# Performance work log

Hardware: AMD Instinct MI355X
Metric: run time of the kernel (lower is better)

The kernel has to match this reference:

```python
import jax, jax.numpy as jnp
import numpy as np

CAUSAL = True

def setup_inputs() -> dict:
    key = jax.random.key(0)
    kq, kk, kv = jax.random.split(key, 3)
    B, S, H, D = 2, 2048, 16, 64
    q = jax.random.normal(kq, (B, S, H, D), dtype=jnp.float32)
    k = jax.random.normal(kk, (B, S, H, D), dtype=jnp.float32)
    v = jax.random.normal(kv, (B, S, H, D), dtype=jnp.float32)
    return {"q": q, "k": k, "v": v}

def reference(q, k, v):
    # q,k,v: [B, S, H, D]
    B, Sq, H, D = q.shape
    Sk = k.shape[1]
    scale = 1.0 / jnp.sqrt(jnp.asarray(D, dtype=q.dtype))
    # scores: [B, H, Sq, Sk]
    scores = jnp.einsum('bqhd,bkhd->bhqk', q * scale, k)
    if CAUSAL:
        causal_mask = jnp.triu(jnp.ones((Sq, Sk), dtype=bool), k=1)
        scores = jnp.where(causal_mask, -jnp.inf, scores)
    attn = jax.nn.softmax(scores, axis=-1)
    # output: [B, Sq, H, D]
    out = jnp.einsum('bhqk,bkhd->bqhd', attn, v)
    return out
```

## Files before the change

### kernel.cpp

```cpp
#include <hip/hip_runtime.h>


typedef __bf16  bf16x8_t  __attribute__((ext_vector_type(8)));
typedef short   short8_t  __attribute__((ext_vector_type(8)));
typedef float   f32x4     __attribute__((ext_vector_type(4)));

#define MFMA_K32(a, b, c) __builtin_amdgcn_mfma_f32_16x16x32_bf16((a), (b), (c), 0, 0, 0)
#define BC8(x) __builtin_bit_cast(bf16x8_t, (x))

constexpr int   SEQ = 2048, NH = 16;
constexpr int   SROW = NH * 64;
constexpr float QS   = 0.125f * 1.44269504088896f;

__device__ __forceinline__ unsigned f2bfu(float f) {
    unsigned u = __builtin_bit_cast(unsigned, f);
    return (u + 0x7fffu + ((u >> 16) & 1u)) >> 16;
}
__device__ __forceinline__ unsigned pk2(float x, float y) {
#if defined(__HIP_DEVICE_COMPILE__) && __has_builtin(__builtin_amdgcn_cvt_pk_bf16_f32)
    typedef __bf16 bfv2 __attribute__((ext_vector_type(2)));
    bfv2 v = __builtin_amdgcn_cvt_pk_bf16_f32(x, y);
    return __builtin_bit_cast(unsigned, v);
#else
    return (f2bfu(x) & 0xffffu) | (f2bfu(y) << 16);
#endif
}

__global__ __launch_bounds__(256) void prepack(const float* __restrict__ K,
                                               const float* __restrict__ V,
                                               unsigned short* __restrict__ Kp,
                                               unsigned short* __restrict__ Vp) {
    const int blk = blockIdx.x;
    const int tid = threadIdx.x;
    const int bh = blk >> 5, c = blk & 31;
    const int b  = bh >> 4,  h = bh & 15;

    __shared__ float LK[64][68];
    __shared__ float LV[64][68];

    const float* Ksrc = K + (size_t)(b * SEQ + c * 64) * SROW + h * 64;
    const float* Vsrc = V + (size_t)(b * SEQ + c * 64) * SROW + h * 64;

#pragma unroll
    for (int p = 0; p < 4; ++p) {
        const int f   = p * 256 + tid;
        const int row = f >> 4;
        const int c4  = (f & 15) * 4;
        float4 kk = *(const float4*)(Ksrc + (size_t)row * SROW + c4);
        float4 vv = *(const float4*)(Vsrc + (size_t)row * SROW + c4);
        *(float4*)&LK[row][c4] = kk;
        *(float4*)&LV[row][c4] = vv;
    }
    __syncthreads();

#pragma unroll
    for (int u = tid; u < 512; u += 256) {
        const int q_l = u >> 7, ks = (u >> 6) & 1, lane = u & 63;
        const int lhi = lane >> 4, llo = lane & 15;
        const float* r = &LK[q_l * 16 + llo][ks * 32 + lhi * 8];
        uint4 o;
        o.x = pk2(r[0], r[1]); o.y = pk2(r[2], r[3]);
        o.z = pk2(r[4], r[5]); o.w = pk2(r[6], r[7]);
        *(uint4*)(Kp + (size_t)(bh * 128 + c * 4) * 1024 + u * 8) = o;
    }

#pragma unroll
    for (int u = tid; u < 512; u += 256) {
        const int g_l = u >> 8, dt = (u >> 6) & 3, lane = u & 63;
        const int lhi = lane >> 4, llo = lane & 15;
        const int d   = dt * 16 + llo;
        const int kvb = g_l * 32 + lhi * 4;
        uint4 o;
        o.x = pk2(LV[kvb + 0][d],  LV[kvb + 1][d]);
        o.y = pk2(LV[kvb + 2][d],  LV[kvb + 3][d]);
        o.z = pk2(LV[kvb + 16][d], LV[kvb + 17][d]);
        o.w = pk2(LV[kvb + 18][d], LV[kvb + 19][d]);
        *(uint4*)(Vp + (size_t)(bh * 64 + c * 2) * 2048 + u * 8) = o;
    }
}

__global__ __launch_bounds__(256, 4) void fa_fwd(const float* __restrict__ Q,
                                                 const unsigned short* __restrict__ Kp,
                                                 const unsigned short* __restrict__ Vp,
                                                 float* __restrict__ O) {
    const int id = blockIdx.x;
    const int bh = id & 31;
    const int T  = 63 - (id >> 5);
    const int b  = bh >> 4, h = bh & 15;
    const int NSC = (T + 4) >> 2;
    const int q0  = T * 32;

    const int tid  = threadIdx.x;
    const int w    = tid >> 6;
    const int lane = tid & 63;
    const int lhi  = lane >> 4;
    const int llo  = lane & 15;

    __shared__ __align__(16) float Red[4][5][64][4];

    const char* Ku = (const char*)Kp + ((size_t)bh << 18);
    const char* Vu = (const char*)Vp + ((size_t)bh << 18);
    int kov = (w << 12) + lane * 16;
    int vov = (w << 12) + lane * 16;

    bf16x8_t qf[2][2];
#pragma unroll
    for (int mt = 0; mt < 2; ++mt)
#pragma unroll
        for (int ks = 0; ks < 2; ++ks) {
            const float* qp = Q + (size_t)(b * SEQ + q0 + mt * 16 + llo) * SROW + h * 64 + ks * 32 + lhi * 8;
            float4 a = ((const float4*)qp)[0], c4 = ((const float4*)qp)[1];
            uint4 u;
            u.x = pk2(a.x * QS, a.y * QS); u.y = pk2(a.z * QS, a.w * QS);
            u.z = pk2(c4.x * QS, c4.y * QS); u.w = pk2(c4.z * QS, c4.w * QS);
            qf[mt][ks] = __builtin_bit_cast(bf16x8_t, u);
        }

    f32x4 acc[2][4], accL[2];
#pragma unroll
    for (int mt = 0; mt < 2; ++mt) {
        accL[mt] = (f32x4){0.f, 0.f, 0.f, 0.f};
#pragma unroll
        for (int dt = 0; dt < 4; ++dt) acc[mt][dt] = (f32x4){0.f, 0.f, 0.f, 0.f};
    }

    short8_t o8;
#pragma unroll
    for (int j = 0; j < 8; ++j) o8[j] = (short)0x3F80;
    const bf16x8_t ones8 = __builtin_bit_cast(bf16x8_t, o8);

    uint4 kc[4];
#pragma unroll
    for (int i = 0; i < 4; ++i) kc[i] = *(const uint4*)(Ku + kov + i * 1024);

    for (int sc = 0; sc < NSC; ++sc) {
        uint4 vc[4];
#pragma unroll
        for (int dt = 0; dt < 4; ++dt) vc[dt] = *(const uint4*)(Vu + vov + dt * 1024);

        const int kb = (sc << 7) + (w << 5);

        __builtin_amdgcn_s_setprio(1);
        f32x4 s00 = (f32x4){0.f, 0.f, 0.f, 0.f};
        f32x4 s01 = (f32x4){0.f, 0.f, 0.f, 0.f};
        f32x4 s10 = (f32x4){0.f, 0.f, 0.f, 0.f};
        f32x4 s11 = (f32x4){0.f, 0.f, 0.f, 0.f};
        s00 = MFMA_K32(BC8(kc[0]), qf[0][0], s00);
        s10 = MFMA_K32(BC8(kc[0]), qf[1][0], s10);
        s01 = MFMA_K32(BC8(kc[2]), qf[0][0], s01);
        s11 = MFMA_K32(BC8(kc[2]), qf[1][0], s11);
        s00 = MFMA_K32(BC8(kc[1]), qf[0][1], s00);
        s10 = MFMA_K32(BC8(kc[1]), qf[1][1], s10);
        s01 = MFMA_K32(BC8(kc[3]), qf[0][1], s01);
        s11 = MFMA_K32(BC8(kc[3]), qf[1][1], s11);
        __builtin_amdgcn_s_setprio(0);

        kov += 16384;
#pragma unroll
        for (int i = 0; i < 4; ++i) kc[i] = *(const uint4*)(Ku + kov + i * 1024);

        {
            const int m_g0 = q0 + llo;
            if (kb + 15 > q0) {
#pragma unroll
                for (int r = 0; r < 4; ++r)
                    if (kb + lhi * 4 + r > m_g0) s00[r] = -INFINITY;
            }
            if (kb + 31 > q0) {
#pragma unroll
                for (int r = 0; r < 4; ++r)
                    if (kb + 16 + lhi * 4 + r > m_g0) s01[r] = -INFINITY;
            }
            const int m1  = q0 + 16;
            const int m_g1 = m1 + llo;
            if (kb + 15 > m1) {
#pragma unroll
                for (int r = 0; r < 4; ++r)
                    if (kb + lhi * 4 + r > m_g1) s10[r] = -INFINITY;
            }
            if (kb + 31 > m1) {
#pragma unroll
                for (int r = 0; r < 4; ++r)
                    if (kb + 16 + lhi * 4 + r > m_g1) s11[r] = -INFINITY;
            }
        }

        uint4 up0, up1;
        up0.x = pk2(__builtin_amdgcn_exp2f(s00[0]), __builtin_amdgcn_exp2f(s00[1]));
        up0.y = pk2(__builtin_amdgcn_exp2f(s00[2]), __builtin_amdgcn_exp2f(s00[3]));
        up0.z = pk2(__builtin_amdgcn_exp2f(s01[0]), __builtin_amdgcn_exp2f(s01[1]));
        up0.w = pk2(__builtin_amdgcn_exp2f(s01[2]), __builtin_amdgcn_exp2f(s01[3]));
        up1.x = pk2(__builtin_amdgcn_exp2f(s10[0]), __builtin_amdgcn_exp2f(s10[1]));
        up1.y = pk2(__builtin_amdgcn_exp2f(s10[2]), __builtin_amdgcn_exp2f(s10[3]));
        up1.z = pk2(__builtin_amdgcn_exp2f(s11[0]), __builtin_amdgcn_exp2f(s11[1]));
        up1.w = pk2(__builtin_amdgcn_exp2f(s11[2]), __builtin_amdgcn_exp2f(s11[3]));
        const bf16x8_t pf0 = BC8(up0);
        const bf16x8_t pf1 = BC8(up1);

        __builtin_amdgcn_s_setprio(1);
#pragma unroll
        for (int dt = 0; dt < 4; ++dt) {
            acc[0][dt] = MFMA_K32(pf0, BC8(vc[dt]), acc[0][dt]);
            acc[1][dt] = MFMA_K32(pf1, BC8(vc[dt]), acc[1][dt]);
        }
        accL[0] = MFMA_K32(pf0, ones8, accL[0]);
        accL[1] = MFMA_K32(pf1, ones8, accL[1]);
        __builtin_amdgcn_s_setprio(0);

        vov += 16384;
    }

#pragma unroll
    for (int mt = 0; mt < 2; ++mt) {
#pragma unroll
        for (int dt = 0; dt < 4; ++dt) *(f32x4*)&Red[w][dt][lane][0] = acc[mt][dt];
        *(f32x4*)&Red[w][4][lane][0] = accL[mt];
        __syncthreads();
        f32x4 oc = (f32x4){0.f, 0.f, 0.f, 0.f};
        f32x4 ls = (f32x4){0.f, 0.f, 0.f, 0.f};
#pragma unroll
        for (int u = 0; u < 4; ++u) {
            oc += *(const f32x4*)&Red[u][w][lane][0];
            ls += *(const f32x4*)&Red[u][4][lane][0];
        }
#pragma unroll
        for (int r = 0; r < 4; ++r)
            O[(size_t)(b * SEQ + q0 + mt * 16 + lhi * 4 + r) * SROW + h * 64 + w * 16 + llo] = oc[r] / ls[r];
        __syncthreads();
    }
}

extern "C" void kernel_launch(void* const* d_in, const int* in_sizes, int n_in,
                              void* d_out, int out_size, void* d_ws, size_t ws_size,
                              hipStream_t stream) {
    const float* q = (const float*)d_in[0];
    const float* k = (const float*)d_in[1];
    const float* v = (const float*)d_in[2];
    float* o = (float*)d_out;
    unsigned short* Kp = (unsigned short*)d_ws;
    unsigned short* Vp = Kp + (size_t)32 * 32 * 4096;
    prepack<<<dim3(1024), dim3(256), 0, stream>>>(k, v, Kp, Vp);
    fa_fwd<<<dim3(2048), dim3(256), 0, stream>>>(q, Kp, Vp, o);
}
```

Before: 123.6 us.

## Stage K/V tiles in LDS via async global_load_lds double buffering with warp-split work

Replaces per-wave direct register loads of K/V with block-wide async global-to-LDS loads into a double-buffered shared tile, so each 64-key chunk is fetched once per block and shared by all four waves. Waves are re-split as two query m-tiles times two key halves, which halves per-wave register state, so the occupancy hint is raised from 4 to 5. Waves whose rows are fully masked skip the work, and the final reduction reuses the LDS buffer and multiplies by a reciprocal. It adds a __syncthreads per iteration and smaller per-iteration work, which risks sync overhead, and the prefetch on the last iteration reads one chunk past the end.

```diff
diff --git a/kernel.cpp b/kernel.cpp
--- a/kernel.cpp
+++ b/kernel.cpp
@@ -23,6 +23,14 @@
     return __builtin_bit_cast(unsigned, v);
 #else
     return (f2bfu(x) & 0xffffu) | (f2bfu(y) << 16);
+#endif
+}
+
+__device__ __forceinline__ void gload_lds16(const void* g, void* l) {
+#if defined(__HIP_DEVICE_COMPILE__)
+    __builtin_amdgcn_global_load_lds(
+        (const __attribute__((address_space(1))) unsigned*)g,
+        (__attribute__((address_space(3))) unsigned*)l, 16, 0, 0);
 #endif
 }
 
@@ -79,7 +87,7 @@
     }
 }
 
-__global__ __launch_bounds__(256, 4) void fa_fwd(const float* __restrict__ Q,
+__global__ __launch_bounds__(256, 5) void fa_fwd(const float* __restrict__ Q,
                                                  const unsigned short* __restrict__ Kp,
                                                  const unsigned short* __restrict__ Vp,
                                                  float* __restrict__ O) {
@@ -87,146 +95,141 @@
     const int bh = id & 31;
     const int T  = 63 - (id >> 5);
     const int b  = bh >> 4, h = bh & 15;
-    const int NSC = (T + 4) >> 2;
+    const int NSC = (T >> 1) + 1;
     const int q0  = T * 32;
 
     const int tid  = threadIdx.x;
     const int w    = tid >> 6;
+    const int mt   = w >> 1;
+    const int kvh  = w & 1;
     const int lane = tid & 63;
     const int lhi  = lane >> 4;
     const int llo  = lane & 15;
 
-    __shared__ __align__(16) float Red[4][5][64][4];
+    __shared__ __align__(16) uint4 KV[2][1024];
 
     const char* Ku = (const char*)Kp + ((size_t)bh << 18);
     const char* Vu = (const char*)Vp + ((size_t)bh << 18);
-    int kov = (w << 12) + lane * 16;
-    int vov = (w << 12) + lane * 16;
-
-    bf16x8_t qf[2][2];
-#pragma unroll
-    for (int mt = 0; mt < 2; ++mt)
-#pragma unroll
-        for (int ks = 0; ks < 2; ++ks) {
-            const float* qp = Q + (size_t)(b * SEQ + q0 + mt * 16 + llo) * SROW + h * 64 + ks * 32 + lhi * 8;
-            float4 a = ((const float4*)qp)[0], c4 = ((const float4*)qp)[1];
-            uint4 u;
-            u.x = pk2(a.x * QS, a.y * QS); u.y = pk2(a.z * QS, a.w * QS);
-            u.z = pk2(c4.x * QS, c4.y * QS); u.w = pk2(c4.z * QS, c4.w * QS);
-            qf[mt][ks] = __builtin_bit_cast(bf16x8_t, u);
-        }
-
-    f32x4 acc[2][4], accL[2];
-#pragma unroll
-    for (int mt = 0; mt < 2; ++mt) {
-        accL[mt] = (f32x4){0.f, 0.f, 0.f, 0.f};
-#pragma unroll
-        for (int dt = 0; dt < 4; ++dt) acc[mt][dt] = (f32x4){0.f, 0.f, 0.f, 0.f};
-    }
+
+    bf16x8_t qf[2];
+#pragma unroll
+    for (int ks = 0; ks < 2; ++ks) {
+        const float* qp = Q + (size_t)(b * SEQ + q0 + mt * 16 + llo) * SROW + h * 64 + ks * 32 + lhi * 8;
+        float4 a = ((const float4*)qp)[0], c4 = ((const float4*)qp)[1];
+        uint4 u;
+        u.x = pk2(a.x * QS, a.y * QS); u.y = pk2(a.z * QS, a.w * QS);
+        u.z = pk2(c4.x * QS, c4.y * QS); u.w = pk2(c4.z * QS, c4.w * QS);
+        qf[ks] = __builtin_bit_cast(bf16x8_t, u);
+    }
+
+    f32x4 acc[4], accL;
+    accL = (f32x4){0.f, 0.f, 0.f, 0.f};
+#pragma unroll
+    for (int dt = 0; dt < 4; ++dt) acc[dt] = (f32x4){0.f, 0.f, 0.f, 0.f};
 
     short8_t o8;
 #pragma unroll
     for (int j = 0; j < 8; ++j) o8[j] = (short)0x3F80;
     const bf16x8_t ones8 = __builtin_bit_cast(bf16x8_t, o8);
 
-    uint4 kc[4];
-#pragma unroll
-    for (int i = 0; i < 4; ++i) kc[i] = *(const uint4*)(Ku + kov + i * 1024);
+    const int m0  = q0 + mt * 16;
+    const int m_g = m0 + llo;
+    const int myEnd = ((m0 + 15 - (kvh << 5)) >> 6) + 1;
+    const int kb0   = kvh << 5;
+
+    {
+        const char* ks0 = Ku + tid * 16;
+        const char* vs0 = Vu + tid * 16;
+        gload_lds16(ks0,        &KV[0][tid]);
+        gload_lds16(ks0 + 4096, &KV[0][tid + 256]);
+        gload_lds16(vs0,        &KV[0][tid + 512]);
+        gload_lds16(vs0 + 4096, &KV[0][tid + 768]);
+    }
+    __syncthreads();
 
     for (int sc = 0; sc < NSC; ++sc) {
-        uint4 vc[4];
-#pragma unroll
-        for (int dt = 0; dt < 4; ++dt) vc[dt] = *(const uint4*)(Vu + vov + dt * 1024);
-
-        const int kb = (sc << 7) + (w << 5);
-
-        __builtin_amdgcn_s_setprio(1);
-        f32x4 s00 = (f32x4){0.f, 0.f, 0.f, 0.f};
-        f32x4 s01 = (f32x4){0.f, 0.f, 0.f, 0.f};
-        f32x4 s10 = (f32x4){0.f, 0.f, 0.f, 0.f};
-        f32x4 s11 = (f32x4){0.f, 0.f, 0.f, 0.f};
-        s00 = MFMA_K32(BC8(kc[0]), qf[0][0], s00);
-        s10 = MFMA_K32(BC8(kc[0]), qf[1][0], s10);
-        s01 = MFMA_K32(BC8(kc[2]), qf[0][0], s01);
-        s11 = MFMA_K32(BC8(kc[2]), qf[1][0], s11);
-        s00 = MFMA_K32(BC8(kc[1]), qf[0][1], s00);
-        s10 = MFMA_K32(BC8(kc[1]), qf[1][1], s10);
-        s01 = MFMA_K32(BC8(kc[3]), qf[0][1], s01);
-        s11 = MFMA_K32(BC8(kc[3]), qf[1][1], s11);
-        __builtin_amdgcn_s_setprio(0);
-
-        kov += 16384;
-#pragma unroll
-        for (int i = 0; i < 4; ++i) kc[i] = *(const uint4*)(Ku + kov + i * 1024);
+        const int cb = sc & 1, nb = cb ^ 1;
 
         {
-            const int m_g0 = q0 + llo;
-            if (kb + 15 > q0) {
+            const char* ksrc = Ku + (size_t)(sc + 1) * 8192 + tid * 16;
+            const char* vsrc = Vu + (size_t)(sc + 1) * 8192 + tid * 16;
+            gload_lds16(ksrc,        &KV[nb][tid]);
+            gload_lds16(ksrc + 4096, &KV[nb][tid + 256]);
+            gload_lds16(vsrc,        &KV[nb][tid + 512]);
+            gload_lds16(vsrc + 4096, &KV[nb][tid + 768]);
+        }
+
+        if (sc < myEnd) {
+            const int kbase = (kvh << 8) + lane;
+            uint4 kc0 = KV[cb][kbase];
+            uint4 kc1 = KV[cb][kbase + 64];
+            uint4 kc2 = KV[cb][kbase + 128];
+            uint4 kc3 = KV[cb][kbase + 192];
+            uint4 vc0 = KV[cb][kbase + 512];
+            uint4 vc1 = KV[cb][kbase + 576];
+            uint4 vc2 = KV[cb][kbase + 640];
+            uint4 vc3 = KV[cb][kbase + 704];
+
+            __builtin_amdgcn_s_setprio(1);
+            f32x4 s0 = (f32x4){0.f, 0.f, 0.f, 0.f};
+            f32x4 s1 = (f32x4){0.f, 0.f, 0.f, 0.f};
+            s0 = MFMA_K32(BC8(kc0), qf[0], s0);
+            s1 = MFMA_K32(BC8(kc2), qf[0], s1);
+            s0 = MFMA_K32(BC8(kc1), qf[1], s0);
+            s1 = MFMA_K32(BC8(kc3), qf[1], s1);
+            __builtin_amdgcn_s_setprio(0);
+
+            const int kb = (sc << 6) + kb0;
+            if (kb + 15 > m0) {
 #pragma unroll
                 for (int r = 0; r < 4; ++r)
-                    if (kb + lhi * 4 + r > m_g0) s00[r] = -INFINITY;
+                    if (kb + lhi * 4 + r > m_g) s0[r] = -INFINITY;
             }
-            if (kb + 31 > q0) {
+            if (kb + 31 > m0) {
 #pragma unroll
                 for (int r = 0; r < 4; ++r)
-                    if (kb + 16 + lhi * 4 + r > m_g0) s01[r] = -INFINITY;
+                    if (kb + 16 + lhi * 4 + r > m_g) s1[r] = -INFINITY;
             }
-            const int m1  = q0 + 16;
-            const int m_g1 = m1 + llo;
-            if (kb + 15 > m1) {
-#pragma unroll
-                for (int r = 0; r < 4; ++r)
-                    if (kb + lhi * 4 + r > m_g1) s10[r] = -INFINITY;
-            }
-            if (kb + 31 > m1) {
-#pragma unroll
-                for (int r = 0; r < 4; ++r)
-                    if (kb + 16 + lhi * 4 + r > m_g1) s11[r] = -INFINITY;
-            }
+
+            uint4 up;
+            up.x = pk2(__builtin_amdgcn_exp2f(s0[0]), __builtin_amdgcn_exp2f(s0[1]));
+            up.y = pk2(__builtin_amdgcn_exp2f(s0[2]), __builtin_amdgcn_exp2f(s0[3]));
+            up.z = pk2(__builtin_amdgcn_exp2f(s1[0]), __builtin_amdgcn_exp2f(s1[1]));
+            up.w = pk2(__builtin_amdgcn_exp2f(s1[2]), __builtin_amdgcn_exp2f(s1[3]));
+            const bf16x8_t pf = BC8(up);
+
+            __builtin_amdgcn_s_setprio(1);
+            acc[0] = MFMA_K32(pf, BC8(vc0), acc[0]);
+            acc[1] = MFMA_K32(pf, BC8(vc1), acc[1]);
+            acc[2] = MFMA_K32(pf, BC8(vc2), acc[2]);
+            acc[3] = MFMA_K32(pf, BC8(vc3), acc[3]);
+            accL   = MFMA_K32(pf, ones8, accL);
+            __builtin_amdgcn_s_setprio(0);
         }
 
-        uint4 up0, up1;
-        up0.x = pk2(__builtin_amdgcn_exp2f(s00[0]), __builtin_amdgcn_exp2f(s00[1]));
-        up0.y = pk2(__builtin_amdgcn_exp2f(s00[2]), __builtin_amdgcn_exp2f(s00[3]));
-        up0.z = pk2(__builtin_amdgcn_exp2f(s01[0]), __builtin_amdgcn_exp2f(s01[1]));
-        up0.w = pk2(__builtin_amdgcn_exp2f(s01[2]), __builtin_amdgcn_exp2f(s01[3]));
-        up1.x = pk2(__builtin_amdgcn_exp2f(s10[0]), __builtin_amdgcn_exp2f(s10[1]));
-        up1.y = pk2(__builtin_amdgcn_exp2f(s10[2]), __builtin_amdgcn_exp2f(s10[3]));
-        up1.z = pk2(__builtin_amdgcn_exp2f(s11[0]), __builtin_amdgcn_exp2f(s11[1]));
-        up1.w = pk2(__builtin_amdgcn_exp2f(s11[2]), __builtin_amdgcn_exp2f(s11[3]));
-        const bf16x8_t pf0 = BC8(up0);
-        const bf16x8_t pf1 = BC8(up1);
-
-        __builtin_amdgcn_s_setprio(1);
-#pragma unroll
-        for (int dt = 0; dt < 4; ++dt) {
-            acc[0][dt] = MFMA_K32(pf0, BC8(vc[dt]), acc[0][dt]);
-            acc[1][dt] = MFMA_K32(pf1, BC8(vc[dt]), acc[1][dt]);
-        }
-        accL[0] = MFMA_K32(pf0, ones8, accL[0]);
-        accL[1] = MFMA_K32(pf1, ones8, accL[1]);
-        __builtin_amdgcn_s_setprio(0);
-
-        vov += 16384;
-    }
-
-#pragma unroll
-    for (int mt = 0; mt < 2; ++mt) {
-#pragma unroll
-        for (int dt = 0; dt < 4; ++dt) *(f32x4*)&Red[w][dt][lane][0] = acc[mt][dt];
-        *(f32x4*)&Red[w][4][lane][0] = accL[mt];
         __syncthreads();
-        f32x4 oc = (f32x4){0.f, 0.f, 0.f, 0.f};
-        f32x4 ls = (f32x4){0.f, 0.f, 0.f, 0.f};
-#pragma unroll
-        for (int u = 0; u < 4; ++u) {
-            oc += *(const f32x4*)&Red[u][w][lane][0];
-            ls += *(const f32x4*)&Red[u][4][lane][0];
-        }
+    }
+
+    typedef float RedT[5][64][4];
+    RedT* Red = (RedT*)(void*)KV;
+#pragma unroll
+    for (int dt = 0; dt < 4; ++dt) *(f32x4*)&Red[w][dt][lane][0] = acc[dt];
+    *(f32x4*)&Red[w][4][lane][0] = accL;
+    __syncthreads();
+
+    const int wa = mt << 1, wb = wa + 1;
+    f32x4 ls = *(const f32x4*)&Red[wa][4][lane][0] + *(const f32x4*)&Red[wb][4][lane][0];
+    f32x4 inv;
+#pragma unroll
+    for (int r = 0; r < 4; ++r) inv[r] = 1.0f / ls[r];
+
+#pragma unroll
+    for (int i = 0; i < 2; ++i) {
+        const int dt = (kvh << 1) + i;
+        f32x4 oc = *(const f32x4*)&Red[wa][dt][lane][0] + *(const f32x4*)&Red[wb][dt][lane][0];
 #pragma unroll
         for (int r = 0; r < 4; ++r)
-            O[(size_t)(b * SEQ + q0 + mt * 16 + lhi * 4 + r) * SROW + h * 64 + w * 16 + llo] = oc[r] / ls[r];
-        __syncthreads();
+            O[(size_t)(b * SEQ + q0 + mt * 16 + lhi * 4 + r) * SROW + h * 64 + dt * 16 + llo] = oc[r] * inv[r];
     }
 }
 
```

Measured after the change: 125.1 us. Within noise of the previous version (+1.3%).
